# Optimization experiments

Measured on AMD Instinct MI355X. Metric: run time of the kernel, lower is better.

The kernel has to match this reference:

```python
import jax, jax.numpy as jnp
import numpy as np

B, L = 1, 320
CS, CZ, CH, H, PQ, PV = 384, 128, 16, 12, 4, 8
INF, EPS = 1e5, 1e-8


def _quat_to_rot(q):
    w, x, y, z = q[..., 0], q[..., 1], q[..., 2], q[..., 3]
    r0 = jnp.stack([1 - 2*(y*y + z*z), 2*(x*y - w*z), 2*(x*z + w*y)], -1)
    r1 = jnp.stack([2*(x*y + w*z), 1 - 2*(x*x + z*z), 2*(y*z - w*x)], -1)
    r2 = jnp.stack([2*(x*z - w*y), 2*(y*z + w*x), 1 - 2*(x*x + y*y)], -1)
    return jnp.stack([r0, r1, r2], -2)


def setup_inputs():
    key = jax.random.key(0)
    ks = jax.random.split(key, 12)

    def lin(k, fan_in, fan_out):
        k1, k2 = jax.random.split(k)
        lim = 1.0 / np.sqrt(fan_in)
        return (jax.random.uniform(k1, (fan_in, fan_out), minval=-lim, maxval=lim, dtype=jnp.float32),
                jax.random.uniform(k2, (fan_out,), minval=-lim, maxval=lim, dtype=jnp.float32))

    s = jax.random.normal(ks[0], (B, L, CS), dtype=jnp.float32)
    quat = jax.random.normal(ks[1], (B, L, 4), dtype=jnp.float32)
    quat = quat / jnp.linalg.norm(quat, axis=-1, keepdims=True)
    rot = _quat_to_rot(quat)                                   # proper rotations (B,L,3,3)
    trans = 10.0 * jax.random.normal(ks[2], (B, L, 3), dtype=jnp.float32)
    z = jax.random.normal(ks[3], (B, L, L, CZ), dtype=jnp.float32)
    frame_mask = jnp.ones((B, L), dtype=jnp.float32)

    Wq, bq = lin(ks[4], CS, CH * H)
    Wkv, bkv = lin(ks[5], CS, 2 * CH * H)
    Wqp, bqp = lin(ks[6], CS, 6 * H * PQ)
    Wkvp, bkvp = lin(ks[7], CS, 6 * H * (PQ + PV))
    Wg, bg = lin(ks[8], CS, H * PQ)
    geom_weights = jnp.ones((3,), jnp.float32)
    dir_weight = jnp.asarray(0.5, jnp.float32)
    head_weights = 0.02 * jax.random.normal(ks[9], (H,), dtype=jnp.float32)
    concat_dim = H * (CH + 7 * PV) + H * CZ                    # 2400
    Wo, bo = lin(ks[10], concat_dim, CS)
    return dict(s=s, rot=rot, trans=trans, z=z, frame_mask=frame_mask,
                Wq=Wq, bq=bq, Wkv=Wkv, bkv=bkv, Wqp=Wqp, bqp=bqp,
                Wkvp=Wkvp, bkvp=bkvp, Wg=Wg, bg=bg,
                geom_weights=geom_weights, dir_weight=dir_weight,
                head_weights=head_weights, Wo=Wo, bo=bo)


def reference(s, rot, trans, z, frame_mask, Wq, bq, Wkv, bkv, Wqp, bqp,
              Wkvp, bkvp, Wg, bg, geom_weights, dir_weight, head_weights, Wo, bo):
    def proc_pts(pts_flat, P):
        # (B,L,6*H*P) -> rotate coords+translate, rotate dirs -> (B,L,H,P,6)
        pts = pts_flat.reshape(B, L, H, P, 6)
        coords = jnp.einsum('blij,blhpj->blhpi', rot, pts[..., :3]) + trans[:, :, None, None, :]
        dirs = jnp.einsum('blij,blhpj->blhpi', rot, pts[..., 3:])
        return jnp.concatenate([coords, dirs], -1)

    q = (s @ Wq + bq).reshape(B, L, H, CH)
    kv = s @ Wkv + bkv
    k = kv[..., :CH * H].reshape(B, L, H, CH)
    v = kv[..., CH * H:].reshape(B, L, H, CH)

    q_pts = proc_pts(s @ Wqp + bqp, PQ)
    kv_pts = s @ Wkvp + bkvp
    k_pts = proc_pts(kv_pts[..., :6 * H * PQ], PQ)
    v_pts = proc_pts(kv_pts[..., 6 * H * PQ:], PV)

    gate = jax.nn.sigmoid(s @ Wg + bg).reshape(B, L, H, PQ, 1)
    q_pts = q_pts * gate

    scalar_att = jnp.einsum('bqhc,bkhc->bhqk', q, k) / np.sqrt(CH).astype(np.float32)

    # position attention: per-pair point distances + log + inverse, mean over points
    delta = q_pts[:, :, None, :, :, :3] - k_pts[:, None, :, :, :, :3]   # (B,Lq,Lk,H,PQ,3)
    d = jnp.linalg.norm(delta, axis=-1)
    pos_att = (d + jnp.log(d + EPS) + 1.0 / (d + EPS)).mean(-1).transpose(0, 3, 1, 2)

    # direction attention: per-point dot minus cross-product 'curvature'
    qd, kd = q_pts[..., 3:], k_pts[..., 3:]
    dot = jnp.einsum('bqhpd,bkhpd->bqkhp', qd, kd)                       # (B,Lq,Lk,H,P)
    cr = jnp.cross(qd[:, :, None, :, None, :, :], kd[:, None, :, :, :, None, :])  # (B,Lq,Lk,H,Pk,Pq,3)
    cross = jnp.linalg.norm(cr, axis=-1).mean(-1)                        # (B,Lq,Lk,H,Pk)
    nq = jnp.linalg.norm(qd, axis=-1)[:, :, None]                        # (B,Lq,1,H,P)
    nk = jnp.linalg.norm(kd, axis=-1)[:, None]                           # (B,1,Lk,H,P)
    dir_att = (dot - cross / (nq * nk + EPS)).mean(-1).transpose(0, 3, 1, 2)

    att = scalar_att + dir_weight * (geom_weights[0] * pos_att + geom_weights[1] * dir_att)
    att = att * head_weights[:, None, None]
    mask2d = frame_mask[:, None, None, :] * frame_mask[:, None, :, None]  # (B,1,L,L)
    att = jax.nn.softmax(att + INF * (mask2d - 1.0), axis=-1)

    o_scalar = jnp.einsum('bhqk,bkhc->bqhc', att, v)
    o_geom = jnp.einsum('bhqk,bkhpd->bqhpd', att, v_pts)                 # (B,L,H,PV,6)

    # map aggregated geometry back into local frames
    rotT = jnp.swapaxes(rot, -1, -2)
    trans_inv = -jnp.einsum('blij,blj->bli', rotT, trans)
    lc = jnp.einsum('blij,blhpj->blhpi', rotT, o_geom[..., :3]) + trans_inv[:, :, None, None, :]
    ld = jnp.einsum('blij,blhpj->blhpi', rotT, o_geom[..., 3:6])
    ld = ld / jnp.maximum(jnp.linalg.norm(ld, axis=-1, keepdims=True), 1e-12)  # F.normalize
    ln = jnp.linalg.norm(lc, axis=-1, keepdims=True)
    o_geom7 = jnp.concatenate([lc, ld, ln], -1)                          # (B,L,H,PV,7)

    o_pair = jnp.einsum('bhij,bijk->bihk', att, z)                       # (B,L,H,CZ)
    out = jnp.concatenate([o_scalar.reshape(B, L, H * CH),
                           o_geom7.reshape(B, L, H * PV * 7),
                           o_pair.reshape(B, L, H * CZ)], -1)
    return out @ Wo + bo
```

## Files before the change

kernel.cpp:

```cpp
#include <hip/hip_runtime.h>
#include <hip/hip_bf16.h>
#include <math.h>

#define LSEQ 320
#define CS 384
#define CZ 128
#define CH 16
#define NH 12
#define PQ 4
#define PV 8
#define EPSF 1e-8f

typedef short short8 __attribute__((ext_vector_type(8)));
typedef float f32x4 __attribute__((ext_vector_type(4)));
typedef unsigned short ush2 __attribute__((ext_vector_type(2)));

__device__ __forceinline__ unsigned short f2b(float x) {
    union { float f; unsigned u; } v; v.f = x;
    unsigned r = (v.u + 0x7FFF + ((v.u >> 16) & 1)) >> 16;
    return (unsigned short)r;
}
__device__ __forceinline__ float b2f(unsigned short h) {
    union { unsigned u; float f; } v; v.u = ((unsigned)h) << 16;
    return v.f;
}

#define OFF_Q       0
#define OFF_KV      61440
#define OFF_QPT     184320
#define OFF_SHI     276480
#define OFF_SMID    337920
#define OFF_SLO     399360
#define OFF_ATTHI   552960
#define OFF_PARTG   552960
#define OFF_CCHIS   1167360
#define OFF_CCLOS   1551360
#define OFF_CCHI    2191360
#define OFF_WCATHI  3051520
#define OFF_WCATMID 3392512
#define OFF_WCATLO  3733504
#define OFF_BCAT    4074496
#define OFF_WOHI    4076272
#define OFF_WOLO    4537072
#define OFF_QPR     5243632
#define OFF_KVPR    5335792
#define OFF_GATE    5612272
#define OFF_PART    5627632
#define OFF_KROW    6242032
#define OFF_WCTHI   6426352
#define OFF_WCTMID  6767344
#define OFF_WCTLO   7108336
#define OFF_WOTHI   7449328
#define OFF_WOTLO   7910128

__global__ __launch_bounds__(256) void k_cast(
    const float* __restrict__ s,
    const float* __restrict__ Wq, const float* __restrict__ bq,
    const float* __restrict__ Wkv, const float* __restrict__ bkv,
    const float* __restrict__ Wqp, const float* __restrict__ bqp,
    const float* __restrict__ Wkvp, const float* __restrict__ bkvp,
    const float* __restrict__ Wg, const float* __restrict__ bg,
    const float* __restrict__ Wo,
    unsigned short* __restrict__ s_hi, unsigned short* __restrict__ s_mid,
    unsigned short* __restrict__ s_lo,
    unsigned short* __restrict__ w_hi, unsigned short* __restrict__ w_mid,
    unsigned short* __restrict__ w_lo,
    float* __restrict__ bcat,
    unsigned short* __restrict__ wo_hi, unsigned short* __restrict__ wo_lo)
{
    int i = blockIdx.x * 256 + threadIdx.x;
    if (i < 122880) {
        float x = s[i];
        unsigned short hi = f2b(x);
        float r1 = x - b2f(hi);
        unsigned short mid = f2b(r1);
        s_hi[i] = hi; s_mid[i] = mid; s_lo[i] = f2b(r1 - b2f(mid));
        return;
    }
    i -= 122880;
    if (i < 681984) {
        int k = i / 1776, c = i - k * 1776;
        float v;
        if (c < 192)       v = Wq[(size_t)k * 192 + c];
        else if (c < 576)  v = Wkv[(size_t)k * 384 + c - 192];
        else if (c < 864)  v = Wqp[(size_t)k * 288 + c - 576];
        else if (c < 1728) v = Wkvp[(size_t)k * 864 + c - 864];
        else               v = Wg[(size_t)k * 48 + c - 1728];
        unsigned short hi = f2b(v);
        float r1 = v - b2f(hi);
        unsigned short mid = f2b(r1);
        w_hi[i] = hi; w_mid[i] = mid; w_lo[i] = f2b(r1 - b2f(mid));
        return;
    }
    i -= 681984;
    if (i < 1776) {
        float v;
        if (i < 192)       v = bq[i];
        else if (i < 576)  v = bkv[i - 192];
        else if (i < 864)  v = bqp[i - 576];
        else if (i < 1728) v = bkvp[i - 864];
        else               v = bg[i - 1728];
        bcat[i] = v;
        return;
    }
    i -= 1776;
    if (i < 921600) {
        float v = Wo[i];
        unsigned short hi = f2b(v);
        wo_hi[i] = hi; wo_lo[i] = f2b(v - b2f(hi));
        return;
    }
}

__global__ __launch_bounds__(256) void k_tr(
    const unsigned short* __restrict__ wc_hi, const unsigned short* __restrict__ wc_mid,
    const unsigned short* __restrict__ wc_lo,
    const unsigned short* __restrict__ wo_hi, const unsigned short* __restrict__ wo_lo,
    unsigned short* __restrict__ wcT_hi, unsigned short* __restrict__ wcT_mid,
    unsigned short* __restrict__ wcT_lo,
    unsigned short* __restrict__ woT_hi, unsigned short* __restrict__ woT_lo)
{
    int m = blockIdx.z;
    const unsigned short* in; unsigned short* outp; int R, C;
    if (m == 0)      { in = wc_hi;  outp = wcT_hi;  R = 384;  C = 1776; }
    else if (m == 1) { in = wc_mid; outp = wcT_mid; R = 384;  C = 1776; }
    else if (m == 2) { in = wc_lo;  outp = wcT_lo;  R = 384;  C = 1776; }
    else if (m == 3) { in = wo_hi;  outp = woT_hi;  R = 2400; C = 384;  }
    else             { in = wo_lo;  outp = woT_lo;  R = 2400; C = 384;  }
    int r0 = blockIdx.x * 64, c0 = blockIdx.y * 64;
    if (r0 >= R || c0 >= C) return;
    __shared__ unsigned short t[64][65];
    int tid = threadIdx.x;
    #pragma unroll
    for (int rep = 0; rep < 16; rep++) {
        int idx = rep * 256 + tid;
        int i = idx >> 6, j = idx & 63;
        if (r0 + i < R && c0 + j < C) t[i][j] = in[(size_t)(r0 + i) * C + c0 + j];
    }
    __syncthreads();
    #pragma unroll
    for (int rep = 0; rep < 16; rep++) {
        int idx = rep * 256 + tid;
        int i = idx >> 6, j = idx & 63;
        if (c0 + i < C && r0 + j < R) outp[(size_t)(c0 + i) * R + r0 + j] = t[j][i];
    }
}

__global__ __launch_bounds__(192) void k_proj(
    const unsigned short* __restrict__ s_hi, const unsigned short* __restrict__ s_mid,
    const unsigned short* __restrict__ s_lo,
    const unsigned short* __restrict__ wcT_hi, const unsigned short* __restrict__ wcT_mid,
    const unsigned short* __restrict__ wcT_lo,
    const float* __restrict__ bcat,
    float* __restrict__ qo, float* __restrict__ kvo,
    float* __restrict__ qpr, float* __restrict__ kvpr, float* __restrict__ gate)
{
    __shared__ unsigned short a_h[16][56], a_m[16][56], a_l[16][56];
    __shared__ unsigned short w_h[48][56], w_m[48][56], w_l[48][56];
    int col0 = blockIdx.x * 48, l0 = blockIdx.y * 16;
    int tid = threadIdx.x;
    int lane = tid & 63, w = tid >> 6;
    int ncol = lane & 15, blk = lane >> 4, mrow = (lane >> 4) * 4;

    float* dst; int nc, cbase; bool sig = false;
    if (col0 < 192)       { nc = 192; cbase = col0;        dst = qo;   }
    else if (col0 < 576)  { nc = 384; cbase = col0 - 192;  dst = kvo;  }
    else if (col0 < 864)  { nc = 288; cbase = col0 - 576;  dst = qpr;  }
    else if (col0 < 1728) { nc = 864; cbase = col0 - 864;  dst = kvpr; }
    else                  { nc = 48;  cbase = 0;           dst = gate; sig = true; }

    f32x4 acc = {};
    for (int k0 = 0; k0 < 384; k0 += 32) {
        __syncthreads();
        {
            int arr = tid >> 6, idx = tid & 63;
            int row = idx >> 2, seg = idx & 3;
            size_t off = (size_t)(l0 + row) * 384 + k0 + seg * 8;
            if (arr == 0)      *(short8*)&a_h[row][seg * 8] = *(const short8*)(s_hi + off);
            else if (arr == 1) *(short8*)&a_m[row][seg * 8] = *(const short8*)(s_mid + off);
            else               *(short8*)&a_l[row][seg * 8] = *(const short8*)(s_lo + off);
        }
        {
            int row = tid >> 2, seg = tid & 3;
            size_t off = (size_t)(col0 + row) * 384 + k0 + seg * 8;
            *(short8*)&w_h[row][seg * 8] = *(const short8*)(wcT_hi + off);
            *(short8*)&w_m[row][seg * 8] = *(const short8*)(wcT_mid + off);
            *(short8*)&w_l[row][seg * 8] = *(const short8*)(wcT_lo + off);
        }
        __syncthreads();
        short8 afh = *(short8*)&a_h[ncol][blk * 8];
        short8 afm = *(short8*)&a_m[ncol][blk * 8];
        short8 afl = *(short8*)&a_l[ncol][blk * 8];
        short8 bfh = *(short8*)&w_h[w * 16 + ncol][blk * 8];
        short8 bfm = *(short8*)&w_m[w * 16 + ncol][blk * 8];
        short8 bfl = *(short8*)&w_l[w * 16 + ncol][blk * 8];
        acc = __builtin_amdgcn_mfma_f32_16x16x32_bf16(afm, bfm, acc, 0, 0, 0);
        acc = __builtin_amdgcn_mfma_f32_16x16x32_bf16(afh, bfl, acc, 0, 0, 0);
        acc = __builtin_amdgcn_mfma_f32_16x16x32_bf16(afl, bfh, acc, 0, 0, 0);
        acc = __builtin_amdgcn_mfma_f32_16x16x32_bf16(afh, bfm, acc, 0, 0, 0);
        acc = __builtin_amdgcn_mfma_f32_16x16x32_bf16(afm, bfh, acc, 0, 0, 0);
        acc = __builtin_amdgcn_mfma_f32_16x16x32_bf16(afh, bfh, acc, 0, 0, 0);
    }
    {
        int n = w * 16 + ncol;
        float bv = bcat[col0 + n];
        int cloc = cbase + n;
        #pragma unroll
        for (int r = 0; r < 4; r++) {
            float v2 = acc[r] + bv;
            if (sig) v2 = 1.0f / (1.0f + expf(-v2));
            dst[(size_t)(l0 + mrow + r) * nc + cloc] = v2;
        }
    }
}

__global__ __launch_bounds__(256) void k_points(
    const float* __restrict__ qpr, const float* __restrict__ kvpr, const float* __restrict__ gate,
    const float* __restrict__ rot, const float* __restrict__ trans,
    const float* __restrict__ kv,
    float* __restrict__ qpt, float* __restrict__ krow,
    float* __restrict__ vpt)
{
    __shared__ float kp_s[48][6];
    __shared__ float kn_s[48];
    int l = blockIdx.x, t = threadIdx.x;
    const float* R = rot + l * 9;
    float tx = trans[l * 3], ty = trans[l * 3 + 1], tz = trans[l * 3 + 2];
    if (t < 192) {
        const float* src; float g = 1.0f; float* dst = nullptr; int vj = -1, kj = -1;
        if (t < 48)      { src = qpr + (size_t)l * 288 + t * 6; g = gate[l * 48 + t]; dst = qpt + ((size_t)l * 48 + t) * 6; }
        else if (t < 96) { kj = t - 48; src = kvpr + (size_t)l * 864 + kj * 6; }
        else             { int j = t - 96; src = kvpr + (size_t)l * 864 + 288 + j * 6; vj = j; }
        float px = src[0], py = src[1], pz = src[2], ux = src[3], uy = src[4], uz = src[5];
        float c0 = R[0] * px + R[1] * py + R[2] * pz + tx;
        float c1 = R[3] * px + R[4] * py + R[5] * pz + ty;
        float c2 = R[6] * px + R[7] * py + R[8] * pz + tz;
        float d0 = R[0] * ux + R[1] * uy + R[2] * uz;
        float d1 = R[3] * ux + R[4] * uy + R[5] * uz;
        float d2 = R[6] * ux + R[7] * uy + R[8] * uz;
        if (vj >= 0) {
            float* vd = vpt + (size_t)l * 576 + vj * 6;
            vd[0] = c0; vd[1] = c1; vd[2] = c2;
            vd[3] = d0; vd[4] = d1; vd[5] = d2;
        } else if (kj >= 0) {
            kp_s[kj][0] = c0; kp_s[kj][1] = c1; kp_s[kj][2] = c2;
            kp_s[kj][3] = d0; kp_s[kj][4] = d1; kp_s[kj][5] = d2;
            kn_s[kj] = sqrtf(d0 * d0 + d1 * d1 + d2 * d2);
        } else {
            dst[0] = c0 * g; dst[1] = c1 * g; dst[2] = c2 * g;
            dst[3] = d0 * g; dst[4] = d1 * g; dst[5] = d2 * g;
        }
    }
    __syncthreads();
    for (int idx = t; idx < 576; idx += 256) {
        int h = idx / 48, j = idx - h * 48;
        float v;
        if (j < 24)      v = kp_s[h * 4 + j / 6][j % 6];
        else if (j < 40) v = kv[(size_t)l * 384 + h * 16 + (j - 24)];
        else if (j < 44) v = kn_s[h * 4 + (j - 40)];
        else             v = 0.0f;
        krow[((size_t)h * 320 + l) * 48 + j] = v;
    }
}

__global__ __launch_bounds__(256) void k_att(
    const float* __restrict__ qb, const float* __restrict__ qpt,
    const float* __restrict__ krow,
    const float* __restrict__ fm, const float* __restrict__ gw,
    const float* __restrict__ dwp, const float* __restrict__ hwp,
    float* __restrict__ att)
{
    int tid = threadIdx.x;
    int w = tid >> 6, lane = tid & 63;
    int iqA = blockIdx.x * 8 + w * 2;
    int iqB = iqA + 1;
    int h = blockIdx.y;

    float qvA[CH], qvB[CH];
    #pragma unroll
    for (int c = 0; c < CH; c++) {
        qvA[c] = qb[(size_t)iqA * 192 + h * CH + c];
        qvB[c] = qb[(size_t)iqB * 192 + h * CH + c];
    }
    float qpA[24], qpB[24];
    #pragma unroll
    for (int j = 0; j < 24; j++) {
        qpA[j] = qpt[(size_t)iqA * 288 + h * 24 + j];
        qpB[j] = qpt[(size_t)iqB * 288 + h * 24 + j];
    }
    float nqA[PQ], nq2A[PQ], nqB[PQ], nq2B[PQ];
    #pragma unroll
    for (int p = 0; p < PQ; p++) {
        float x = qpA[p * 6 + 3], y = qpA[p * 6 + 4], zz = qpA[p * 6 + 5];
        nq2A[p] = x * x + y * y + zz * zz; nqA[p] = sqrtf(nq2A[p]);
        x = qpB[p * 6 + 3]; y = qpB[p * 6 + 4]; zz = qpB[p * 6 + 5];
        nq2B[p] = x * x + y * y + zz * zz; nqB[p] = sqrtf(nq2B[p]);
    }
    float dwv = dwp[0], g0 = gw[0], g1 = gw[1], hwv = hwp[h];
    float fmA = fm[iqA], fmB = fm[iqB];

    float lgA[5], lgB[5];
    for (int r = 0; r < 5; r++) {
        int kk = r * 64 + lane;
        const float* rowp = krow + ((size_t)h * 320 + kk) * 48;
        float rw[44];
        #pragma unroll
        for (int j = 0; j < 44; j++) rw[j] = rowp[j];
        float fmk = fm[kk];

        #pragma unroll
        for (int which = 0; which < 2; which++) {
            const float* qp = which ? qpB : qpA;
            const float* qv = which ? qvB : qvA;
            const float* nq = which ? nqB : nqA;
            const float* nq2 = which ? nq2B : nq2A;
            float fmi = which ? fmB : fmA;

            float scalar = 0.f;
            #pragma unroll
            for (int c = 0; c < CH; c++) scalar += qv[c] * rw[24 + c];
            scalar *= 0.25f;

            float pos = 0.f;
            #pragma unroll
            for (int p = 0; p < PQ; p++) {
                float dx = qp[p * 6] - rw[p * 6];
                float dy = qp[p * 6 + 1] - rw[p * 6 + 1];
                float dz = qp[p * 6 + 2] - rw[p * 6 + 2];
                float d = __builtin_amdgcn_sqrtf(dx * dx + dy * dy + dz * dz);
                float de = d + EPSF;
                pos += d + __logf(de) + __builtin_amdgcn_rcpf(de);
            }
            pos *= 0.25f;

            float dir = 0.f;
            #pragma unroll
            for (int p = 0; p < PQ; p++) {
                float kx = rw[p * 6 + 3], ky = rw[p * 6 + 4], kz = rw[p * 6 + 5];
                float nk = rw[40 + p];
                float nk2 = nk * nk;
                float cm = 0.f, dself = 0.f;
                #pragma unroll
                for (int pq = 0; pq < PQ; pq++) {
                    float dq = qp[pq * 6 + 3] * kx + qp[pq * 6 + 4] * ky + qp[pq * 6 + 5] * kz;
                    if (pq == p) dself = dq;
                    cm += __builtin_amdgcn_sqrtf(fmaxf(nq2[pq] * nk2 - dq * dq, 0.0f));
                }
                cm *= 0.25f;
                dir += dself - cm * __builtin_amdgcn_rcpf(nq[p] * nk + EPSF);
            }
            dir *= 0.25f;

            float logit = scalar + dwv * (g0 * pos + g1 * dir);
            logit *= hwv;
            logit += 100000.0f * (fmi * fmk - 1.0f);
            if (which) lgB[r] = logit; else lgA[r] = logit;
        }
    }

    float mxA = lgA[0];
    #pragma unroll
    for (int r = 1; r < 5; r++) mxA = fmaxf(mxA, lgA[r]);
    for (int m = 32; m; m >>= 1) mxA = fmaxf(mxA, __shfl_xor(mxA, m, 64));
    float eA[5], smA = 0.f;
    #pragma unroll
    for (int r = 0; r < 5; r++) { eA[r] = __expf(lgA[r] - mxA); smA += eA[r]; }
    for (int m = 32; m; m >>= 1) smA += __shfl_xor(smA, m, 64);
    float invA = 1.0f / smA;
    #pragma unroll
    for (int r = 0; r < 5; r++)
        att[((size_t)h * 320 + iqA) * 320 + r * 64 + lane] = eA[r] * invA;
    float mxB = lgB[0];
    #pragma unroll
    for (int r = 1; r < 5; r++) mxB = fmaxf(mxB, lgB[r]);
    for (int m = 32; m; m >>= 1) mxB = fmaxf(mxB, __shfl_xor(mxB, m, 64));
    float eB[5], smB = 0.f;
    #pragma unroll
    for (int r = 0; r < 5; r++) { eB[r] = __expf(lgB[r] - mxB); smB += eB[r]; }
    for (int m = 32; m; m >>= 1) smB += __shfl_xor(smB, m, 64);
    float invB = 1.0f / smB;
    #pragma unroll
    for (int r = 0; r < 5; r++)
        att[((size_t)h * 320 + iqB) * 320 + r * 64 + lane] = eB[r] * invB;
}

__global__ __launch_bounds__(256) void k_sv_simple(
    const float* __restrict__ att,
    const float* __restrict__ kv,
    const float* __restrict__ vpt,
    const float* __restrict__ rot, const float* __restrict__ trans,
    float* __restrict__ cc)
{
    __shared__ float a_s[12][320];
    __shared__ float og[576];
    int iq = blockIdx.x, tid = threadIdx.x;
    for (int j = tid; j < 12 * 320; j += 256) {
        int h = j / 320, k = j - h * 320;
        a_s[h][k] = att[((size_t)h * 320 + iq) * 320 + k];
    }
    __syncthreads();
    for (int j = tid; j < 768; j += 256) {
        float acc = 0.f;
        if (j < 192) {
            int h = j >> 4;
            for (int k = 0; k < 320; k++)
                acc += a_s[h][k] * kv[(size_t)k * 384 + 192 + j];
            cc[(size_t)iq * 2400 + j] = acc;
        } else {
            int jg = j - 192;
            int h = jg / 48;
            for (int k = 0; k < 320; k++)
                acc += a_s[h][k] * vpt[(size_t)k * 576 + jg];
            og[jg] = acc;
        }
    }
    __syncthreads();
    if (tid < 96) {
        const float* R = rot + iq * 9;
        float tx = trans[iq * 3], ty = trans[iq * 3 + 1], tz = trans[iq * 3 + 2];
        const float* o = &og[tid * 6];
        float gx = o[0] - tx, gy = o[1] - ty, gz = o[2] - tz;
        float l0 = R[0] * gx + R[3] * gy + R[6] * gz;
        float l1 = R[1] * gx + R[4] * gy + R[7] * gz;
        float l2 = R[2] * gx + R[5] * gy + R[8] * gz;
        float dx = o[3], dy = o[4], dz = o[5];
        float e0 = R[0] * dx + R[3] * dy + R[6] * dz;
        float e1 = R[1] * dx + R[4] * dy + R[7] * dz;
        float e2 = R[2] * dx + R[5] * dy + R[8] * dz;
        float n = sqrtf(e0 * e0 + e1 * e1 + e2 * e2);
        float inv = 1.0f / fmaxf(n, 1e-12f);
        float ln = sqrtf(l0 * l0 + l1 * l1 + l2 * l2);
        float vals[7] = { l0, l1, l2, e0 * inv, e1 * inv, e2 * inv, ln };
        size_t base = (size_t)iq * 2400 + 192 + tid * 7;
        #pragma unroll
        for (int j = 0; j < 7; j++) cc[base + j] = vals[j];
    }
}

__global__ __launch_bounds__(256) void k_pair(
    const float* __restrict__ att,
    const float* __restrict__ z,
    float* __restrict__ cc)
{
    __shared__ unsigned short a_hi[16][56];
    __shared__ unsigned short a_lo[16][56];
    __shared__ unsigned short B[128][56];
    int iq = blockIdx.x, tid = threadIdx.x;
    int lane = tid & 63, w = tid >> 6;
    int ncol = lane & 15, blk = lane >> 4, mrow = (lane >> 4) * 4;

    f32x4 acc[2] = {};
    for (int k0 = 0; k0 < 320; k0 += 32) {
        __syncthreads();
        {
            int row = tid >> 4, c2 = (tid & 15) * 2;
            float v0 = 0.f, v1 = 0.f;
            if (row < 12) {
                const float* ap = att + ((size_t)row * 320 + iq) * 320 + k0 + c2;
                v0 = ap[0]; v1 = ap[1];
            }
            ush2 h2, l2;
            h2[0] = f2b(v0); l2[0] = f2b(v0 - b2f(h2[0]));
            h2[1] = f2b(v1); l2[1] = f2b(v1 - b2f(h2[1]));
            *(ush2*)&a_hi[row][c2] = h2;
            *(ush2*)&a_lo[row][c2] = l2;
        }
        {
            int kp2 = (tid & 15) * 2;
            int cb = (tid >> 4) * 8;
            const float* src0 = z + ((size_t)iq * 320 + k0 + kp2) * 128 + cb;
            float4 a0 = *(const float4*)(src0);
            float4 a1 = *(const float4*)(src0 + 4);
            float4 b0 = *(const float4*)(src0 + 128);
            float4 b1 = *(const float4*)(src0 + 132);
            float va[8] = {a0.x, a0.y, a0.z, a0.w, a1.x, a1.y, a1.z, a1.w};
            float vb[8] = {b0.x, b0.y, b0.z, b0.w, b1.x, b1.y, b1.z, b1.w};
            #pragma unroll
            for (int c = 0; c < 8; c++) {
                ush2 pr;
                pr[0] = f2b(va[c]);
                pr[1] = f2b(vb[c]);
                *(ush2*)&B[cb + c][kp2] = pr;
            }
        }
        __syncthreads();
        short8 afh = *(short8*)&a_hi[ncol][blk * 8];
        short8 afl = *(short8*)&a_lo[ncol][blk * 8];
        #pragma unroll
        for (int s2 = 0; s2 < 2; s2++) {
            short8 bf = *(short8*)&B[w * 32 + s2 * 16 + ncol][blk * 8];
            acc[s2] = __builtin_amdgcn_mfma_f32_16x16x32_bf16(afl, bf, acc[s2], 0, 0, 0);
            acc[s2] = __builtin_amdgcn_mfma_f32_16x16x32_bf16(afh, bf, acc[s2], 0, 0, 0);
        }
    }
    #pragma unroll
    for (int s2 = 0; s2 < 2; s2++) {
        int n = w * 32 + s2 * 16 + ncol;
        #pragma unroll
        for (int r = 0; r < 4; r++) {
            int h = mrow + r;
            if (h < 12)
                cc[(size_t)iq * 2400 + 864 + (size_t)h * 128 + n] = acc[s2][r];
        }
    }
}

__global__ __launch_bounds__(256) void k_ccsplit(
    const float* __restrict__ cc,
    unsigned short* __restrict__ cc_hi, unsigned short* __restrict__ cc_lo)
{
    int i = blockIdx.x * 256 + threadIdx.x;
    float v = cc[i];
    unsigned short hi = f2b(v);
    cc_hi[i] = hi;
    cc_lo[i] = f2b(v - b2f(hi));
}

__global__ __launch_bounds__(256) void k_gemm(
    const unsigned short* __restrict__ cc_hi, const unsigned short* __restrict__ cc_lo,
    const unsigned short* __restrict__ woT_hi, const unsigned short* __restrict__ woT_lo,
    float* __restrict__ part)
{
    __shared__ unsigned short a_h[16][56], a_l[16][56];
    __shared__ unsigned short w_h[64][56], w_l[64][56];
    int iq0 = blockIdx.x * 16, col0 = blockIdx.y * 64, ks = blockIdx.z;
    int tid = threadIdx.x;
    int lane = tid & 63, w = tid >> 6;
    int ncol = lane & 15, blk = lane >> 4, mrow = (lane >> 4) * 4;

    f32x4 acc = {};
    for (int kc = 0; kc < 15; kc++) {
        int k0 = ks * 480 + kc * 32;
        __syncthreads();
        if (tid < 128) {
            int arr = tid >> 6, idx = tid & 63;
            int row = idx >> 2, seg = idx & 3;
            size_t off = (size_t)(iq0 + row) * 2400 + k0 + seg * 8;
            if (arr == 0) *(short8*)&a_h[row][seg * 8] = *(const short8*)(cc_hi + off);
            else          *(short8*)&a_l[row][seg * 8] = *(const short8*)(cc_lo + off);
        }
        #pragma unroll
        for (int t2 = 0; t2 < 2; t2++) {
            int idx = tid * 2 + t2;
            int arr = idx >> 8, i2 = idx & 255;
            int row = i2 >> 2, seg = i2 & 3;
            size_t off = (size_t)(col0 + row) * 2400 + k0 + seg * 8;
            if (arr == 0) *(short8*)&w_h[row][seg * 8] = *(const short8*)(woT_hi + off);
            else          *(short8*)&w_l[row][seg * 8] = *(const short8*)(woT_lo + off);
        }
        __syncthreads();
        short8 afh = *(short8*)&a_h[ncol][blk * 8];
        short8 afl = *(short8*)&a_l[ncol][blk * 8];
        short8 bfh = *(short8*)&w_h[w * 16 + ncol][blk * 8];
        short8 bfl = *(short8*)&w_l[w * 16 + ncol][blk * 8];
        acc = __builtin_amdgcn_mfma_f32_16x16x32_bf16(afh, bfh, acc, 0, 0, 0);
        acc = __builtin_amdgcn_mfma_f32_16x16x32_bf16(afh, bfl, acc, 0, 0, 0);
        acc = __builtin_amdgcn_mfma_f32_16x16x32_bf16(afl, bfh, acc, 0, 0, 0);
    }
    {
        int cn = col0 + w * 16 + ncol;
        #pragma unroll
        for (int r = 0; r < 4; r++)
            part[((size_t)ks * 320 + iq0 + mrow + r) * 384 + cn] = acc[r];
    }
}

__global__ __launch_bounds__(256) void k_reduce(
    const float* __restrict__ part, const float* __restrict__ bo, float* __restrict__ out)
{
    int i = blockIdx.x * 256 + threadIdx.x;
    float v = bo[i % CS];
    #pragma unroll
    for (int ks = 0; ks < 5; ks++) v += part[(size_t)ks * 122880 + i];
    out[i] = v;
}

extern "C" void kernel_launch(void* const* d_in, const int* in_sizes, int n_in,
                              void* d_out, int out_size, void* d_ws, size_t ws_size,
                              hipStream_t stream)
{
    const float* s     = (const float*)d_in[0];
    const float* rot   = (const float*)d_in[1];
    const float* trans = (const float*)d_in[2];
    const float* z     = (const float*)d_in[3];
    const float* fm    = (const float*)d_in[4];
    const float* Wq    = (const float*)d_in[5];
    const float* bq    = (const float*)d_in[6];
    const float* Wkv   = (const float*)d_in[7];
    const float* bkv   = (const float*)d_in[8];
    const float* Wqp   = (const float*)d_in[9];
    const float* bqp   = (const float*)d_in[10];
    const float* Wkvp  = (const float*)d_in[11];
    const float* bkvp  = (const float*)d_in[12];
    const float* Wg    = (const float*)d_in[13];
    const float* bg    = (const float*)d_in[14];
    const float* gw    = (const float*)d_in[15];
    const float* dw    = (const float*)d_in[16];
    const float* hw    = (const float*)d_in[17];
    const float* Wo    = (const float*)d_in[18];
    const float* bo    = (const float*)d_in[19];

    float* ws = (float*)d_ws;
    float*          q       = ws + OFF_Q;
    float*          kv      = ws + OFF_KV;
    float*          qpt     = ws + OFF_QPT;
    float*          att     = ws + OFF_ATTHI;
    float*          part    = ws + OFF_PARTG;
    unsigned short* cc_hi   = (unsigned short*)(ws + OFF_CCHIS);
    unsigned short* cc_lo   = (unsigned short*)(ws + OFF_CCLOS);
    float*          cc      = ws + OFF_CCHI;
    unsigned short* s_hi    = (unsigned short*)(ws + OFF_SHI);
    unsigned short* s_mid   = (unsigned short*)(ws + OFF_SMID);
    unsigned short* s_lo    = (unsigned short*)(ws + OFF_SLO);
    unsigned short* wc_hi   = (unsigned short*)(ws + OFF_WCATHI);
    unsigned short* wc_mid  = (unsigned short*)(ws + OFF_WCATMID);
    unsigned short* wc_lo   = (unsigned short*)(ws + OFF_WCATLO);
    float*          bcat    = ws + OFF_BCAT;
    unsigned short* wo_hi   = (unsigned short*)(ws + OFF_WOHI);
    unsigned short* wo_lo   = (unsigned short*)(ws + OFF_WOLO);
    float*          qpr     = ws + OFF_QPR;
    float*          kvpr    = ws + OFF_KVPR;
    float*          gate    = ws + OFF_GATE;
    float*          vpt     = ws + OFF_PART;
    float*          krow    = ws + OFF_KROW;
    unsigned short* wcT_hi  = (unsigned short*)(ws + OFF_WCTHI);
    unsigned short* wcT_mid = (unsigned short*)(ws + OFF_WCTMID);
    unsigned short* wcT_lo  = (unsigned short*)(ws + OFF_WCTLO);
    unsigned short* woT_hi  = (unsigned short*)(ws + OFF_WOTHI);
    unsigned short* woT_lo  = (unsigned short*)(ws + OFF_WOTLO);
    float* out = (float*)d_out;

    k_cast<<<dim3(6751), dim3(256), 0, stream>>>(s, Wq, bq, Wkv, bkv, Wqp, bqp,
                                                 Wkvp, bkvp, Wg, bg, Wo,
                                                 s_hi, s_mid, s_lo, wc_hi, wc_mid, wc_lo,
                                                 bcat, wo_hi, wo_lo);
    k_tr<<<dim3(38, 28, 5), dim3(256), 0, stream>>>(wc_hi, wc_mid, wc_lo, wo_hi, wo_lo,
                                                    wcT_hi, wcT_mid, wcT_lo, woT_hi, woT_lo);
    k_proj<<<dim3(37, 20), dim3(192), 0, stream>>>(s_hi, s_mid, s_lo, wcT_hi, wcT_mid, wcT_lo,
                                                   bcat, q, kv, qpr, kvpr, gate);
    k_points<<<dim3(LSEQ), dim3(256), 0, stream>>>(qpr, kvpr, gate, rot, trans, kv,
                                                   qpt, krow, vpt);
    k_att<<<dim3(40, NH), dim3(256), 0, stream>>>(q, qpt, krow, fm, gw, dw, hw, att);
    k_sv_simple<<<dim3(LSEQ), dim3(256), 0, stream>>>(att, kv, vpt, rot, trans, cc);
    k_pair<<<dim3(LSEQ), dim3(256), 0, stream>>>(att, z, cc);
    k_ccsplit<<<dim3(3000), dim3(256), 0, stream>>>(cc, cc_hi, cc_lo);
    k_gemm<<<dim3(20, 6, 5), dim3(256), 0, stream>>>(cc_hi, cc_lo, woT_hi, woT_lo, part);
    k_reduce<<<dim3(480), dim3(256), 0, stream>>>(part, bo, out);
}
```

Measured before the change: 239.0 us.

## Compute attention-value aggregation with split-bf16 MFMA instead of scalar loops

```diff
diff --git a/kernel.cpp b/kernel.cpp
--- a/kernel.cpp
+++ b/kernel.cpp
@@ -42,10 +42,11 @@
 #define OFF_BCAT    4074496
 #define OFF_WOHI    4076272
 #define OFF_WOLO    4537072
+#define OFF_VKVHI   4997872
+#define OFF_VKVLO   5120752
 #define OFF_QPR     5243632
 #define OFF_KVPR    5335792
 #define OFF_GATE    5612272
-#define OFF_PART    5627632
 #define OFF_KROW    6242032
 #define OFF_WCTHI   6426352
 #define OFF_WCTMID  6767344
@@ -219,8 +220,9 @@
     const float* __restrict__ rot, const float* __restrict__ trans,
     const float* __restrict__ kv,
     float* __restrict__ qpt, float* __restrict__ krow,
-    float* __restrict__ vpt)
-{
+    unsigned short* __restrict__ vkv_hi, unsigned short* __restrict__ vkv_lo)
+{
+    __shared__ float vsh[96][6];
     __shared__ float kp_s[48][6];
     __shared__ float kn_s[48];
     int l = blockIdx.x, t = threadIdx.x;
@@ -239,9 +241,8 @@
         float d1 = R[3] * ux + R[4] * uy + R[5] * uz;
         float d2 = R[6] * ux + R[7] * uy + R[8] * uz;
         if (vj >= 0) {
-            float* vd = vpt + (size_t)l * 576 + vj * 6;
-            vd[0] = c0; vd[1] = c1; vd[2] = c2;
-            vd[3] = d0; vd[4] = d1; vd[5] = d2;
+            vsh[vj][0] = c0; vsh[vj][1] = c1; vsh[vj][2] = c2;
+            vsh[vj][3] = d0; vsh[vj][4] = d1; vsh[vj][5] = d2;
         } else if (kj >= 0) {
             kp_s[kj][0] = c0; kp_s[kj][1] = c1; kp_s[kj][2] = c2;
             kp_s[kj][3] = d0; kp_s[kj][4] = d1; kp_s[kj][5] = d2;
@@ -252,6 +253,18 @@
         }
     }
     __syncthreads();
+    #pragma unroll
+    for (int e = 0; e < 3; e++) {
+        int u = t * 3 + e;
+        int h = u >> 6, n = u & 63;
+        float val;
+        if (n < 16) val = kv[(size_t)l * 384 + 192 + h * 16 + n];
+        else        val = vsh[h * 8 + (n - 16) / 6][(n - 16) % 6];
+        unsigned short hi = f2b(val);
+        size_t idx = ((size_t)h * 64 + n) * 320 + l;
+        vkv_hi[idx] = hi;
+        vkv_lo[idx] = f2b(val - b2f(hi));
+    }
     for (int idx = t; idx < 576; idx += 256) {
         int h = idx / 48, j = idx - h * 48;
         float v;
@@ -384,41 +397,67 @@
         att[((size_t)h * 320 + iqB) * 320 + r * 64 + lane] = eB[r] * invB;
 }
 
-__global__ __launch_bounds__(256) void k_sv_simple(
+__global__ __launch_bounds__(256) void k_sv(
     const float* __restrict__ att,
-    const float* __restrict__ kv,
-    const float* __restrict__ vpt,
+    const unsigned short* __restrict__ vkv_hi, const unsigned short* __restrict__ vkv_lo,
     const float* __restrict__ rot, const float* __restrict__ trans,
     float* __restrict__ cc)
 {
-    __shared__ float a_s[12][320];
-    __shared__ float og[576];
-    int iq = blockIdx.x, tid = threadIdx.x;
-    for (int j = tid; j < 12 * 320; j += 256) {
-        int h = j / 320, k = j - h * 320;
-        a_s[h][k] = att[((size_t)h * 320 + iq) * 320 + k];
+    __shared__ unsigned short a_hi[16][56];
+    __shared__ unsigned short a_lo[16][56];
+    __shared__ unsigned short B[128][56];
+    __shared__ float ogsh[16][49];
+    int bid = blockIdx.x;
+    int iq0 = (bid % 20) * 16, h = bid / 20;
+    int tid = threadIdx.x;
+    int lane = tid & 63, w = tid >> 6;
+    int ncol = lane & 15, blk = lane >> 4, mrow = (lane >> 4) * 4;
+
+    f32x4 acc = {};
+    for (int k0 = 0; k0 < 320; k0 += 32) {
+        __syncthreads();
+        {
+            int row = tid >> 4, c2 = (tid & 15) * 2;
+            const float* ap = att + ((size_t)h * 320 + iq0 + row) * 320 + k0 + c2;
+            float v0 = ap[0], v1 = ap[1];
+            ush2 h2, l2;
+            h2[0] = f2b(v0); l2[0] = f2b(v0 - b2f(h2[0]));
+            h2[1] = f2b(v1); l2[1] = f2b(v1 - b2f(h2[1]));
+            *(ush2*)&a_hi[row][c2] = h2;
+            *(ush2*)&a_lo[row][c2] = l2;
+        }
+        {
+            int row = tid >> 2, seg = tid & 3;
+            size_t off = ((size_t)h * 64 + row) * 320 + k0 + seg * 8;
+            *(short8*)&B[row][seg * 8]      = *(const short8*)(vkv_hi + off);
+            *(short8*)&B[64 + row][seg * 8] = *(const short8*)(vkv_lo + off);
+        }
+        __syncthreads();
+        short8 afh = *(short8*)&a_hi[ncol][blk * 8];
+        short8 afl = *(short8*)&a_lo[ncol][blk * 8];
+        short8 bfh = *(short8*)&B[w * 16 + ncol][blk * 8];
+        short8 bfl = *(short8*)&B[64 + w * 16 + ncol][blk * 8];
+        acc = __builtin_amdgcn_mfma_f32_16x16x32_bf16(afh, bfh, acc, 0, 0, 0);
+        acc = __builtin_amdgcn_mfma_f32_16x16x32_bf16(afh, bfl, acc, 0, 0, 0);
+        acc = __builtin_amdgcn_mfma_f32_16x16x32_bf16(afl, bfh, acc, 0, 0, 0);
+    }
+    {
+        int n = w * 16 + ncol;
+        #pragma unroll
+        for (int r = 0; r < 4; r++) {
+            int iq = iq0 + mrow + r;
+            float v = acc[r];
+            if (n < 16) cc[(size_t)iq * 2400 + h * 16 + n] = v;
+            else        ogsh[mrow + r][n - 16] = v;
+        }
     }
     __syncthreads();
-    for (int j = tid; j < 768; j += 256) {
-        float acc = 0.f;
-        if (j < 192) {
-            int h = j >> 4;
-            for (int k = 0; k < 320; k++)
-                acc += a_s[h][k] * kv[(size_t)k * 384 + 192 + j];
-            cc[(size_t)iq * 2400 + j] = acc;
-        } else {
-            int jg = j - 192;
-            int h = jg / 48;
-            for (int k = 0; k < 320; k++)
-                acc += a_s[h][k] * vpt[(size_t)k * 576 + jg];
-            og[jg] = acc;
-        }
-    }
-    __syncthreads();
-    if (tid < 96) {
-        const float* R = rot + iq * 9;
-        float tx = trans[iq * 3], ty = trans[iq * 3 + 1], tz = trans[iq * 3 + 2];
-        const float* o = &og[tid * 6];
+    if (tid < 128) {
+        int iqr = tid >> 3, p = tid & 7;
+        int l = iq0 + iqr;
+        const float* R = rot + l * 9;
+        float tx = trans[l * 3], ty = trans[l * 3 + 1], tz = trans[l * 3 + 2];
+        const float* o = &ogsh[iqr][p * 6];
         float gx = o[0] - tx, gy = o[1] - ty, gz = o[2] - tz;
         float l0 = R[0] * gx + R[3] * gy + R[6] * gz;
         float l1 = R[1] * gx + R[4] * gy + R[7] * gz;
@@ -431,7 +470,7 @@
         float inv = 1.0f / fmaxf(n, 1e-12f);
         float ln = sqrtf(l0 * l0 + l1 * l1 + l2 * l2);
         float vals[7] = { l0, l1, l2, e0 * inv, e1 * inv, e2 * inv, ln };
-        size_t base = (size_t)iq * 2400 + 192 + tid * 7;
+        size_t base = (size_t)l * 2400 + 192 + (h * PV + p) * 7;
         #pragma unroll
         for (int j = 0; j < 7; j++) cc[base + j] = vals[j];
     }
@@ -618,10 +657,11 @@
     float*          bcat    = ws + OFF_BCAT;
     unsigned short* wo_hi   = (unsigned short*)(ws + OFF_WOHI);
     unsigned short* wo_lo   = (unsigned short*)(ws + OFF_WOLO);
+    unsigned short* vkv_hi  = (unsigned short*)(ws + OFF_VKVHI);
+    unsigned short* vkv_lo  = (unsigned short*)(ws + OFF_VKVLO);
     float*          qpr     = ws + OFF_QPR;
     float*          kvpr    = ws + OFF_KVPR;
     float*          gate    = ws + OFF_GATE;
-    float*          vpt     = ws + OFF_PART;
     float*          krow    = ws + OFF_KROW;
     unsigned short* wcT_hi  = (unsigned short*)(ws + OFF_WCTHI);
     unsigned short* wcT_mid = (unsigned short*)(ws + OFF_WCTMID);
@@ -639,9 +679,9 @@
     k_proj<<<dim3(37, 20), dim3(192), 0, stream>>>(s_hi, s_mid, s_lo, wcT_hi, wcT_mid, wcT_lo,
                                                    bcat, q, kv, qpr, kvpr, gate);
     k_points<<<dim3(LSEQ), dim3(256), 0, stream>>>(qpr, kvpr, gate, rot, trans, kv,
-                                                   qpt, krow, vpt);
+                                                   qpt, krow, vkv_hi, vkv_lo);
     k_att<<<dim3(40, NH), dim3(256), 0, stream>>>(q, qpt, krow, fm, gw, dw, hw, att);
-    k_sv_simple<<<dim3(LSEQ), dim3(256), 0, stream>>>(att, kv, vpt, rot, trans, cc);
+    k_sv<<<dim3(240), dim3(256), 0, stream>>>(att, vkv_hi, vkv_lo, rot, trans, cc);
     k_pair<<<dim3(LSEQ), dim3(256), 0, stream>>>(att, z, cc);
     k_ccsplit<<<dim3(3000), dim3(256), 0, stream>>>(cc, cc_hi, cc_lo);
     k_gemm<<<dim3(20, 6, 5), dim3(256), 0, stream>>>(cc_hi, cc_lo, woT_hi, woT_lo, part);
```

New measurement: 216.0 us. 9.6% less time.
